# Optimization experiments

Measured on AMD Instinct MI355X. Metric: run time of the kernel, lower is better.

The kernel has to match this reference:

```python
import jax, jax.numpy as jnp
import numpy as np

N = 50000          # nodes
E = 800000         # edges (avg degree 16)
F = 128            # in_dim = num_hidden*heads = pred_dim
H = 4              # attention heads per layer
D = 32             # num_hidden (per-head dim)
R = 11             # rel_num
L = 2              # num_layers
SCALE = float(1.0 / np.sqrt(D))


def setup_inputs() -> dict:
    key = jax.random.key(0)
    ks = jax.random.split(key, 16)
    inputs = jax.random.normal(ks[0], (N, F), jnp.float32)
    edge_types = jax.random.randint(ks[1], (E,), 0, R)
    src = jax.random.randint(ks[2], (E,), 0, N)
    dst = jax.random.randint(ks[3], (E,), 0, N)
    centrality = jax.random.uniform(ks[4], (N,), jnp.float32)
    rel_emb = jax.random.normal(ks[5], (R, F), jnp.float32) * 0.1
    # stacked per-layer projection weights (both layers have F -> H*D = F)
    Wq = jax.random.normal(ks[6], (L, F, H * D), jnp.float32) * 0.05
    Wk = jax.random.normal(ks[7], (L, F, H * D), jnp.float32) * 0.05
    Wv = jax.random.normal(ks[8], (L, F, H * D), jnp.float32) * 0.05
    We = jax.random.normal(ks[9], (L, F, H * D), jnp.float32) * 0.05
    bq = jnp.zeros((L, H * D), jnp.float32)
    bk = jnp.zeros((L, H * D), jnp.float32)
    bv = jnp.zeros((L, H * D), jnp.float32)
    be = jnp.zeros((L, H * D), jnp.float32)
    W_out = jax.random.normal(ks[10], (H * D, 1), jnp.float32) * 0.05
    b_out = jnp.zeros((1,), jnp.float32)
    gamma = jnp.ones((1,), jnp.float32)
    beta = jnp.zeros((1,), jnp.float32)
    return {"inputs": inputs, "edge_types": edge_types, "src": src, "dst": dst,
            "centrality": centrality, "rel_emb": rel_emb,
            "Wq": Wq, "bq": bq, "Wk": Wk, "bk": bk, "Wv": Wv, "bv": bv,
            "We": We, "be": be, "W_out": W_out, "b_out": b_out,
            "gamma": gamma, "beta": beta}


def _segment_softmax(score, dst, n):
    # score: [E, H]; softmax over incoming edges of each dst node
    m = jax.ops.segment_max(score, dst, num_segments=n)          # [N, H]
    ex = jnp.exp(score - m[dst])                                  # [E, H]
    s = jax.ops.segment_sum(ex, dst, num_segments=n)              # [N, H]
    return ex / (s[dst] + 1e-9)


def reference(inputs, edge_types, src, dst, centrality, rel_emb,
              Wq, bq, Wk, bk, Wv, bv, We, be, W_out, b_out, gamma, beta):
    h = inputs                                   # [N, F]
    ef = rel_emb[edge_types]                     # [E, pred_dim] relational edge embedding
    for l in range(L):
        q = (h @ Wq[l] + bq[l]).reshape(N, H, D)
        k = (h @ Wk[l] + bk[l]).reshape(N, H, D)
        v = (h @ Wv[l] + bv[l]).reshape(N, H, D)
        e = (ef @ We[l] + be[l]).reshape(E, H, D)
        # edge_mode="add": edge features added to keys/values on each edge
        ke = k[src] + e                           # [E, H, D]
        score = jnp.sum(q[dst] * ke, axis=-1) * SCALE   # [E, H]
        attn = _segment_softmax(score, dst, N)          # [E, H]
        msg = attn[:, :, None] * (v[src] + e)           # [E, H, D]
        agg = jax.ops.segment_sum(msg, dst, num_segments=N)  # [N, H, D]
        # identity residual (in_dim == H*D) + ELU activation
        h = jax.nn.elu(agg.reshape(N, H * D) + h)
    logits = h @ W_out + b_out                    # [N, 1]
    logits = jax.nn.relu((centrality * gamma + beta)[:, None] * logits)
    return logits
```

## Files before the change

kernel.cpp:

```cpp
#include <hip/hip_runtime.h>
#include <hip/hip_bf16.h>
#include <math.h>

#define SCALE_C 0.17677669529663687f
#define CAPP 64

typedef short bf16x8 __attribute__((ext_vector_type(8)));
typedef float f32x4 __attribute__((ext_vector_type(4)));
typedef _Float16 h16x2 __attribute__((ext_vector_type(2)));

__device__ __forceinline__ h16x2 bch2(unsigned u) { return __builtin_bit_cast(h16x2, u); }


__global__ __launch_bounds__(256) void prep_scatter_k(
    const float* __restrict__ Wq, const float* __restrict__ Wk, const float* __restrict__ Wv,
    __hip_bfloat16* __restrict__ wf,
    const float* __restrict__ rel_emb, const float* __restrict__ We, const float* __restrict__ be,
    _Float16* __restrict__ re, int R, int reb,
    const int* __restrict__ dst, const int* __restrict__ src, const int* __restrict__ etype,
    int E, int* __restrict__ cnt, int* __restrict__ bins) {
  int b = blockIdx.x;
  if (b < 48) {
    int tid = b * 256 + threadIdx.x;
    int lane = tid & 63;
    int frag = tid >> 6;
    int ks = frag & 3;
    int ct = (frag >> 2) & 7;
    int mat = frag >> 5;
    int l = mat / 3, m = mat % 3;
    const float* W = ((m == 0) ? Wq : (m == 1) ? Wk : Wv) + (size_t)l * 128 * 128;
    int nn = ct * 16 + (lane & 15);
    int k0 = ks * 32 + (lane >> 4) * 8;
    __hip_bfloat16 tmp[8];
    #pragma unroll
    for (int j = 0; j < 8; ++j) tmp[j] = __float2bfloat16(W[(size_t)(k0 + j) * 128 + nn]);
    *(uint4*)&wf[(size_t)frag * 64 * 8 + (size_t)lane * 8] = *(const uint4*)tmp;
  } else if (b < 48 + reb) {
    int idx = (b - 48) * 256 + threadIdx.x;
    int tot = 2 * R * 128;
    if (idx >= tot) return;
    int c = idx & 127;
    int r = (idx >> 7) % R;
    int l = idx / (R * 128);
    const float* W = We + (size_t)l * 128 * 128;
    float acc = be[l * 128 + c];
    #pragma unroll 4
    for (int kk = 0; kk < 128; ++kk) acc += rel_emb[r * 128 + kk] * W[kk * 128 + c];
    re[idx] = (_Float16)acc;
  } else {
    int e = (b - 48 - reb) * 256 + threadIdx.x;
    if (e < E) {
      int d = dst[e];
      int pos = atomicAdd(&cnt[d], 1);
      if (pos < CAPP) bins[(d << 6) + pos] = src[e] | (etype[e] << 20);
    }
  }
}


__device__ __forceinline__ void qkv_body(
    const float* __restrict__ Xf, const __hip_bfloat16* __restrict__ Xb,
    const __hip_bfloat16* __restrict__ wf,
    const float* __restrict__ bq, const float* __restrict__ bk, const float* __restrict__ bv,
    _Float16* __restrict__ qo, _Float16* __restrict__ kvo, int n, int bid) {
  __shared__ _Float16 kvt[2][32][264];
  int wid = threadIdx.x >> 6;
  int lane = threadIdx.x & 63;
  int row0 = bid * 64 + wid * 32;
  if (row0 >= n) return;
  int cl = lane & 15;
  int quad = lane >> 4;

  bf16x8 afrag[2][4];
  #pragma unroll
  for (int s = 0; s < 2; ++s) {
    int arow = row0 + s * 16 + cl;
    bool av = arow < n;
    if (Xb) {
      const __hip_bfloat16* xr = Xb + (size_t)arow * 128 + quad * 8;
      #pragma unroll
      for (int ks = 0; ks < 4; ++ks) {
        uint4 raw = av ? *(const uint4*)(xr + ks * 32) : make_uint4(0, 0, 0, 0);
        afrag[s][ks] = __builtin_bit_cast(bf16x8, raw);
      }
    } else {
      const float* xr = Xf + (size_t)arow * 128 + quad * 8;
      #pragma unroll
      for (int ks = 0; ks < 4; ++ks) {
        float4 x0 = av ? *(const float4*)(xr + ks * 32)     : make_float4(0.f, 0.f, 0.f, 0.f);
        float4 x1 = av ? *(const float4*)(xr + ks * 32 + 4) : make_float4(0.f, 0.f, 0.f, 0.f);
        union { bf16x8 v; __hip_bfloat16 h[8]; } fu;
        fu.h[0] = __float2bfloat16(x0.x); fu.h[1] = __float2bfloat16(x0.y);
        fu.h[2] = __float2bfloat16(x0.z); fu.h[3] = __float2bfloat16(x0.w);
        fu.h[4] = __float2bfloat16(x1.x); fu.h[5] = __float2bfloat16(x1.y);
        fu.h[6] = __float2bfloat16(x1.z); fu.h[7] = __float2bfloat16(x1.w);
        afrag[s][ks] = fu.v;
      }
    }
  }
  const uint4* wfu = (const uint4*)wf;

  #pragma unroll
  for (int ct = 0; ct < 8; ++ct) {
    f32x4 a0 = {0.f, 0.f, 0.f, 0.f}, a1 = {0.f, 0.f, 0.f, 0.f};
    #pragma unroll
    for (int ks = 0; ks < 4; ++ks) {
      uint4 braw = wfu[((size_t)ct * 4 + ks) * 64 + lane];
      bf16x8 bfr = __builtin_bit_cast(bf16x8, braw);
      a0 = __builtin_amdgcn_mfma_f32_16x16x32_bf16(afrag[0][ks], bfr, a0, 0, 0, 0);
      a1 = __builtin_amdgcn_mfma_f32_16x16x32_bf16(afrag[1][ks], bfr, a1, 0, 0, 0);
    }
    int c = ct * 16 + cl;
    float bb = bq[c];
    #pragma unroll
    for (int r = 0; r < 4; ++r) {
      kvt[wid][quad * 4 + r][c]      = (_Float16)((a0[r] + bb) * SCALE_C);
      kvt[wid][16 + quad * 4 + r][c] = (_Float16)((a1[r] + bb) * SCALE_C);
    }
  }
  {
    const uint4* tsrc = (const uint4*)&kvt[wid][0][0];
    #pragma unroll
    for (int it = 0; it < 8; ++it) {
      int idx = it * 64 + lane;
      int row = idx >> 4, g = idx & 15;
      if (row0 + row < n)
        *(uint4*)&qo[((size_t)(row0 + row)) * 128 + g * 8] = tsrc[row * 33 + g];
    }
  }

  #pragma unroll
  for (int m = 1; m <= 2; ++m) {
    const float* bias = (m == 1) ? bk : bv;
    #pragma unroll
    for (int ct = 0; ct < 8; ++ct) {
      f32x4 a0 = {0.f, 0.f, 0.f, 0.f}, a1 = {0.f, 0.f, 0.f, 0.f};
      #pragma unroll
      for (int ks = 0; ks < 4; ++ks) {
        uint4 braw = wfu[((size_t)(m * 8 + ct) * 4 + ks) * 64 + lane];
        bf16x8 bfr = __builtin_bit_cast(bf16x8, braw);
        a0 = __builtin_amdgcn_mfma_f32_16x16x32_bf16(afrag[0][ks], bfr, a0, 0, 0, 0);
        a1 = __builtin_amdgcn_mfma_f32_16x16x32_bf16(afrag[1][ks], bfr, a1, 0, 0, 0);
      }
      int c = ct * 16 + cl;
      float bb = bias[c];
      int p = 8 * (c >> 2) + (c & 3) + ((m == 2) ? 4 : 0);
      #pragma unroll
      for (int r = 0; r < 4; ++r) {
        kvt[wid][quad * 4 + r][p]      = (_Float16)(a0[r] + bb);
        kvt[wid][16 + quad * 4 + r][p] = (_Float16)(a1[r] + bb);
      }
    }
  }
  {
    const uint4* tsrc = (const uint4*)&kvt[wid][0][0];
    #pragma unroll
    for (int it = 0; it < 16; ++it) {
      int idx = it * 64 + lane;
      int row = idx >> 5, off = idx & 31;
      if (row0 + row < n)
        *(uint4*)&kvo[((size_t)(row0 + row)) * 256 + off * 8] = tsrc[row * 33 + off];
    }
  }
}

__global__ __launch_bounds__(128) void qkv1_k(
    const float* __restrict__ Xf, const __hip_bfloat16* __restrict__ wf,
    const float* __restrict__ bq, const float* __restrict__ bk, const float* __restrict__ bv,
    _Float16* __restrict__ qo, _Float16* __restrict__ kvo, int n) {
  qkv_body(Xf, nullptr, wf, bq, bk, bv, qo, kvo, n, blockIdx.x);
}

__global__ __launch_bounds__(128) void qkv2_k(
    const __hip_bfloat16* __restrict__ Xb, const __hip_bfloat16* __restrict__ wf,
    const float* __restrict__ bq, const float* __restrict__ bk, const float* __restrict__ bv,
    _Float16* __restrict__ qo, _Float16* __restrict__ kvo, int n) {
  qkv_body(nullptr, Xb, wf, bq, bk, bv, qo, kvo, n, blockIdx.x);
}


__global__ __launch_bounds__(256) void edge_k(
    const _Float16* __restrict__ qb, const _Float16* __restrict__ kv,
    const _Float16* __restrict__ re,
    const int* __restrict__ bins, const int* __restrict__ cnt,
    const float* __restrict__ h_in_f, const __hip_bfloat16* __restrict__ h_in_b,
    __hip_bfloat16* __restrict__ h_out_b,
    const float* __restrict__ Wout, const float* __restrict__ bout,
    const float* __restrict__ cent, const float* __restrict__ gamma,
    const float* __restrict__ beta, float* __restrict__ outp, int n) {
  int node = blockIdx.x * 4 + (threadIdx.x >> 6);
  if (node >= n) return;
  int lane = threadIdx.x & 63;
  int j = lane & 15;
  int quarter = lane >> 4;
  int deg = cnt[node];
  deg = deg < CAPP ? deg : CAPP;
  uint nm1 = (uint)(n - 1);

  int pkrow = bins[(node << 6) + lane];

  uint4 qraw = *((const uint4*)(qb + ((size_t)node << 7)) + j);
  h16x2 q01 = bch2(qraw.x), q23 = bch2(qraw.y), q45 = bch2(qraw.z), q67 = bch2(qraw.w);
  float qa0 = (float)q01.x, qa1 = (float)q01.y;
  float qa2 = (float)q23.x, qa3 = (float)q23.y;
  float qa4 = (float)q45.x, qa5 = (float)q45.y;
  float qa6 = (float)q67.x, qa7 = (float)q67.y;

  float ssum = 0.f;
  float acc0 = 0.f, acc1 = 0.f, acc2 = 0.f, acc3 = 0.f;
  float acc4 = 0.f, acc5 = 0.f, acc6 = 0.f, acc7 = 0.f;

  int nit = (deg + 3) >> 2;
  nit = (nit + 1) & ~1;

  const uint4* kvb  = (const uint4*)kv + (uint)(j * 2);
  const uint4* rebp = (const uint4*)re + (uint)j;

  auto loadstage = [&](int pk, uint4& r0, uint4& r1, uint4& rr) {
    uint s = (uint)pk & 0xFFFFFu; s = s < nm1 ? s : nm1;
    uint t = (uint)pk >> 20;
    const uint4* kp = kvb + s * 32u;
    r0 = kp[0];
    r1 = kp[1];
    rr = rebp[t * 16u];
  };
  auto accum = [&](uint4 r0, uint4 r1, uint4 rr, int eidx) {
    h16x2 r01 = bch2(rr.x), r23 = bch2(rr.y), r45 = bch2(rr.z), r67 = bch2(rr.w);
    h16x2 kr01 = bch2(r0.x) + r01;
    h16x2 kr23 = bch2(r0.y) + r23;
    h16x2 kr45 = bch2(r1.x) + r45;
    h16x2 kr67 = bch2(r1.y) + r67;
    h16x2 vr01 = bch2(r0.z) + r01;
    h16x2 vr23 = bch2(r0.w) + r23;
    h16x2 vr45 = bch2(r1.z) + r45;
    h16x2 vr67 = bch2(r1.w) + r67;
    float pA = qa0 * (float)kr01.x;
    pA += qa1 * (float)kr01.y;
    pA += qa2 * (float)kr23.x;
    pA += qa3 * (float)kr23.y;
    float pB = qa4 * (float)kr45.x;
    pB += qa5 * (float)kr45.y;
    pB += qa6 * (float)kr67.x;
    pB += qa7 * (float)kr67.y;
    float p = pA + pB;
    p += __shfl_xor(p, 1);
    p += __shfl_xor(p, 2);
    float w = (eidx < deg) ? __expf(p) : 0.f;
    ssum += w;
    acc0 += w * (float)vr01.x;
    acc1 += w * (float)vr01.y;
    acc2 += w * (float)vr23.x;
    acc3 += w * (float)vr23.y;
    acc4 += w * (float)vr45.x;
    acc5 += w * (float)vr45.y;
    acc6 += w * (float)vr67.x;
    acc7 += w * (float)vr67.y;
  };

  uint4 a0, a1, ar, b0, b1, br;
  loadstage(__shfl(pkrow, quarter), a0, a1, ar);
  loadstage(__shfl(pkrow, 4 + quarter), b0, b1, br);

  for (int i = 0; i < nit; i += 2) {
    bool more = (i + 2) < nit;
    int pkA2 = 0, pkB2 = 0;
    if (more) {
      pkA2 = __shfl(pkrow, (4 * i + 8 + quarter) & 63);
      pkB2 = __shfl(pkrow, (4 * i + 12 + quarter) & 63);
    }
    accum(a0, a1, ar, 4 * i + quarter);
    if (more) loadstage(pkA2, a0, a1, ar);
    accum(b0, b1, br, 4 * i + 4 + quarter);
    if (more) loadstage(pkB2, b0, b1, br);
  }

  ssum += __shfl_xor(ssum, 16); ssum += __shfl_xor(ssum, 32);
  acc0 += __shfl_xor(acc0, 16); acc0 += __shfl_xor(acc0, 32);
  acc1 += __shfl_xor(acc1, 16); acc1 += __shfl_xor(acc1, 32);
  acc2 += __shfl_xor(acc2, 16); acc2 += __shfl_xor(acc2, 32);
  acc3 += __shfl_xor(acc3, 16); acc3 += __shfl_xor(acc3, 32);
  acc4 += __shfl_xor(acc4, 16); acc4 += __shfl_xor(acc4, 32);
  acc5 += __shfl_xor(acc5, 16); acc5 += __shfl_xor(acc5, 32);
  acc6 += __shfl_xor(acc6, 16); acc6 += __shfl_xor(acc6, 32);
  acc7 += __shfl_xor(acc7, 16); acc7 += __shfl_xor(acc7, 32);
  if (quarter != 0) return;

  float inv = __builtin_amdgcn_rcpf(ssum + 1e-9f);
  float4 h0, h1;
  if (h_in_b) {
    uint4 hraw = *((const uint4*)(h_in_b + ((size_t)node << 7)) + j);
    h0.x = __uint_as_float(hraw.x << 16); h0.y = __uint_as_float(hraw.x & 0xffff0000u);
    h0.z = __uint_as_float(hraw.y << 16); h0.w = __uint_as_float(hraw.y & 0xffff0000u);
    h1.x = __uint_as_float(hraw.z << 16); h1.y = __uint_as_float(hraw.z & 0xffff0000u);
    h1.z = __uint_as_float(hraw.w << 16); h1.w = __uint_as_float(hraw.w & 0xffff0000u);
  } else {
    const float4* hrow = (const float4*)h_in_f + ((uint)node * 32u + (uint)(j * 2));
    h0 = hrow[0]; h1 = hrow[1];
  }
  float x0 = acc0 * inv + h0.x;
  float x1 = acc1 * inv + h0.y;
  float x2 = acc2 * inv + h0.z;
  float x3 = acc3 * inv + h0.w;
  float x4 = acc4 * inv + h1.x;
  float x5 = acc5 * inv + h1.y;
  float x6 = acc6 * inv + h1.z;
  float x7 = acc7 * inv + h1.w;
  x0 = x0 > 0.f ? x0 : __expf(x0) - 1.f;
  x1 = x1 > 0.f ? x1 : __expf(x1) - 1.f;
  x2 = x2 > 0.f ? x2 : __expf(x2) - 1.f;
  x3 = x3 > 0.f ? x3 : __expf(x3) - 1.f;
  x4 = x4 > 0.f ? x4 : __expf(x4) - 1.f;
  x5 = x5 > 0.f ? x5 : __expf(x5) - 1.f;
  x6 = x6 > 0.f ? x6 : __expf(x6) - 1.f;
  x7 = x7 > 0.f ? x7 : __expf(x7) - 1.f;
  if (outp == nullptr) {
    union { uint4 u; __hip_bfloat16 hh[8]; } P;
    P.hh[0] = __float2bfloat16(x0); P.hh[1] = __float2bfloat16(x1);
    P.hh[2] = __float2bfloat16(x2); P.hh[3] = __float2bfloat16(x3);
    P.hh[4] = __float2bfloat16(x4); P.hh[5] = __float2bfloat16(x5);
    P.hh[6] = __float2bfloat16(x6); P.hh[7] = __float2bfloat16(x7);
    *((uint4*)(h_out_b + ((size_t)node << 7)) + j) = P.u;
  } else {
    const float4* wrow = (const float4*)Wout + (uint)(j * 2);
    float4 w0 = wrow[0], w1 = wrow[1];
    float pp = x0 * w0.x + x1 * w0.y + x2 * w0.z + x3 * w0.w
             + x4 * w1.x + x5 * w1.y + x6 * w1.z + x7 * w1.w;
    pp += __shfl_xor(pp, 1);
    pp += __shfl_xor(pp, 2);
    pp += __shfl_xor(pp, 4);
    pp += __shfl_xor(pp, 8);
    if (lane == 0) {
      float lg = pp + bout[0];
      lg *= (cent[node] * gamma[0] + beta[0]);
      outp[node] = fmaxf(lg, 0.f);
    }
  }
}


extern "C" void kernel_launch(void* const* d_in, const int* in_sizes, int n_in,
                              void* d_out, int out_size, void* d_ws, size_t ws_size,
                              hipStream_t stream) {
  const float* inputs  = (const float*)d_in[0];
  const int*   etype   = (const int*)d_in[1];
  const int*   src     = (const int*)d_in[2];
  const int*   dst     = (const int*)d_in[3];
  const float* cent    = (const float*)d_in[4];
  const float* rel_emb = (const float*)d_in[5];
  const float* Wq      = (const float*)d_in[6];
  const float* bq      = (const float*)d_in[7];
  const float* Wk      = (const float*)d_in[8];
  const float* bk      = (const float*)d_in[9];
  const float* Wv      = (const float*)d_in[10];
  const float* bv      = (const float*)d_in[11];
  const float* We      = (const float*)d_in[12];
  const float* be      = (const float*)d_in[13];
  const float* Wout    = (const float*)d_in[14];
  const float* bout    = (const float*)d_in[15];
  const float* gamma   = (const float*)d_in[16];
  const float* beta    = (const float*)d_in[17];
  float* out = (float*)d_out;

  const int N = in_sizes[0] / 128;
  const int E = in_sizes[1];
  const int R = in_sizes[5] / 128;

  _Float16* re = (_Float16*)d_ws;
  __hip_bfloat16* hb = (__hip_bfloat16*)(re + 2 * (size_t)R * 128);
  _Float16* qb = (_Float16*)(hb + (size_t)N * 128);
  _Float16* kv = qb + (size_t)N * 128;
  __hip_bfloat16* wf = (__hip_bfloat16*)(kv + (size_t)N * 256);
  int* cnt  = (int*)(wf + 6 * 16384);
  int* bins = cnt + N;

  hipMemsetAsync(cnt, 0, (size_t)N * sizeof(int), stream);

  int reb = (2 * R * 128 + 255) / 256;
  int SB  = (E + 255) / 256;
  prep_scatter_k<<<48 + reb + SB, 256, 0, stream>>>(Wq, Wk, Wv, wf, rel_emb, We, be, re, R, reb,
                                                    dst, src, etype, E, cnt, bins);

  int QB = (N + 63) / 64;
  int eb = (N + 3) / 4;
  qkv1_k<<<QB, 128, 0, stream>>>(inputs, wf, bq, bk, bv, qb, kv, N);
  edge_k<<<eb, 256, 0, stream>>>(qb, kv, re, bins, cnt,
                                 inputs, nullptr, hb,
                                 Wout, bout, cent, gamma, beta, nullptr, N);
  qkv2_k<<<QB, 128, 0, stream>>>(hb, wf + (size_t)3 * 16384,
                                 bq + 128, bk + 128, bv + 128, qb, kv, N);
  edge_k<<<eb, 256, 0, stream>>>(qb, kv, re + (size_t)R * 128, bins, cnt,
                                 nullptr, hb, nullptr,
                                 Wout, bout, cent, gamma, beta, out, N);
}
```

Before: 311.0 us.

## Split QKV projection across three waves and de-interleave KV layout

The QKV kernel now stages a 32-row input tile in shared memory and gives each of three waves one projection (Q, K or V). Previously each wave computed all three for its own 32 rows. The KV buffer layout changes from interleaved per-4-element K/V groups to contiguous K then V halves, and the edge gather loads kp[0] and kp[16] to match. In the edge kernel, loads of the bins, q and residual h rows become nontemporal and are issued early, and bin loads are masked by degree. The aim is more parallel waves and earlier latency hiding. In exchange the gather needs two separate 16-byte loads per edge that sit far apart in memory, and the QKV kernel adds a shared-memory staging pass with a barrier.

```diff
diff --git a/kernel.cpp b/kernel.cpp
--- a/kernel.cpp
+++ b/kernel.cpp
@@ -8,8 +8,14 @@
 typedef short bf16x8 __attribute__((ext_vector_type(8)));
 typedef float f32x4 __attribute__((ext_vector_type(4)));
 typedef _Float16 h16x2 __attribute__((ext_vector_type(2)));
+typedef unsigned u32x4 __attribute__((ext_vector_type(4)));
 
 __device__ __forceinline__ h16x2 bch2(unsigned u) { return __builtin_bit_cast(h16x2, u); }
+
+__device__ __forceinline__ uint4 nt_load16(const void* p) {
+  u32x4 v = __builtin_nontemporal_load((const u32x4*)p);
+  return __builtin_bit_cast(uint4, v);
+}
 
 
 __global__ __launch_bounds__(256) void prep_scatter_k(
@@ -63,115 +69,96 @@
     const __hip_bfloat16* __restrict__ wf,
     const float* __restrict__ bq, const float* __restrict__ bk, const float* __restrict__ bv,
     _Float16* __restrict__ qo, _Float16* __restrict__ kvo, int n, int bid) {
-  __shared__ _Float16 kvt[2][32][264];
-  int wid = threadIdx.x >> 6;
-  int lane = threadIdx.x & 63;
-  int row0 = bid * 64 + wid * 32;
+  __shared__ __attribute__((aligned(16))) __hip_bfloat16 xs[32][136];
+  __shared__ __attribute__((aligned(16))) _Float16 ot[3][32][136];
+  int tid = threadIdx.x;
+  int wid = tid >> 6;
+  int lane = tid & 63;
+  int row0 = bid * 32;
   if (row0 >= n) return;
+
+  for (int idx = tid; idx < 512; idx += 192) {
+    int row = idx >> 4, g = idx & 15;
+    union { uint4 u; __hip_bfloat16 h[8]; } P;
+    P.u = make_uint4(0, 0, 0, 0);
+    if (row0 + row < n) {
+      if (Xb) {
+        P.u = *(const uint4*)(Xb + (size_t)(row0 + row) * 128 + g * 8);
+      } else {
+        const float* xr = Xf + (size_t)(row0 + row) * 128 + g * 8;
+        float4 x0 = *(const float4*)xr;
+        float4 x1 = *(const float4*)(xr + 4);
+        P.h[0] = __float2bfloat16(x0.x); P.h[1] = __float2bfloat16(x0.y);
+        P.h[2] = __float2bfloat16(x0.z); P.h[3] = __float2bfloat16(x0.w);
+        P.h[4] = __float2bfloat16(x1.x); P.h[5] = __float2bfloat16(x1.y);
+        P.h[6] = __float2bfloat16(x1.z); P.h[7] = __float2bfloat16(x1.w);
+      }
+    }
+    *(uint4*)&xs[row][g * 8] = P.u;
+  }
+  __syncthreads();
+
   int cl = lane & 15;
   int quad = lane >> 4;
 
   bf16x8 afrag[2][4];
   #pragma unroll
-  for (int s = 0; s < 2; ++s) {
-    int arow = row0 + s * 16 + cl;
-    bool av = arow < n;
-    if (Xb) {
-      const __hip_bfloat16* xr = Xb + (size_t)arow * 128 + quad * 8;
-      #pragma unroll
-      for (int ks = 0; ks < 4; ++ks) {
-        uint4 raw = av ? *(const uint4*)(xr + ks * 32) : make_uint4(0, 0, 0, 0);
-        afrag[s][ks] = __builtin_bit_cast(bf16x8, raw);
-      }
-    } else {
-      const float* xr = Xf + (size_t)arow * 128 + quad * 8;
-      #pragma unroll
-      for (int ks = 0; ks < 4; ++ks) {
-        float4 x0 = av ? *(const float4*)(xr + ks * 32)     : make_float4(0.f, 0.f, 0.f, 0.f);
-        float4 x1 = av ? *(const float4*)(xr + ks * 32 + 4) : make_float4(0.f, 0.f, 0.f, 0.f);
-        union { bf16x8 v; __hip_bfloat16 h[8]; } fu;
-        fu.h[0] = __float2bfloat16(x0.x); fu.h[1] = __float2bfloat16(x0.y);
-        fu.h[2] = __float2bfloat16(x0.z); fu.h[3] = __float2bfloat16(x0.w);
-        fu.h[4] = __float2bfloat16(x1.x); fu.h[5] = __float2bfloat16(x1.y);
-        fu.h[6] = __float2bfloat16(x1.z); fu.h[7] = __float2bfloat16(x1.w);
-        afrag[s][ks] = fu.v;
-      }
-    }
-  }
+  for (int s = 0; s < 2; ++s)
+    #pragma unroll
+    for (int ks = 0; ks < 4; ++ks)
+      afrag[s][ks] = *(const bf16x8*)&xs[s * 16 + cl][quad * 8 + ks * 32];
+
   const uint4* wfu = (const uint4*)wf;
+  const float* bias = (wid == 0) ? bq : (wid == 1) ? bk : bv;
+  float scl = (wid == 0) ? SCALE_C : 1.0f;
 
   #pragma unroll
   for (int ct = 0; ct < 8; ++ct) {
     f32x4 a0 = {0.f, 0.f, 0.f, 0.f}, a1 = {0.f, 0.f, 0.f, 0.f};
     #pragma unroll
     for (int ks = 0; ks < 4; ++ks) {
-      uint4 braw = wfu[((size_t)ct * 4 + ks) * 64 + lane];
+      uint4 braw = wfu[((size_t)(wid * 8 + ct) * 4 + ks) * 64 + lane];
       bf16x8 bfr = __builtin_bit_cast(bf16x8, braw);
       a0 = __builtin_amdgcn_mfma_f32_16x16x32_bf16(afrag[0][ks], bfr, a0, 0, 0, 0);
       a1 = __builtin_amdgcn_mfma_f32_16x16x32_bf16(afrag[1][ks], bfr, a1, 0, 0, 0);
     }
     int c = ct * 16 + cl;
-    float bb = bq[c];
+    float bb = bias[c];
     #pragma unroll
     for (int r = 0; r < 4; ++r) {
-      kvt[wid][quad * 4 + r][c]      = (_Float16)((a0[r] + bb) * SCALE_C);
-      kvt[wid][16 + quad * 4 + r][c] = (_Float16)((a1[r] + bb) * SCALE_C);
-    }
-  }
-  {
-    const uint4* tsrc = (const uint4*)&kvt[wid][0][0];
+      ot[wid][quad * 4 + r][c]      = (_Float16)((a0[r] + bb) * scl);
+      ot[wid][16 + quad * 4 + r][c] = (_Float16)((a1[r] + bb) * scl);
+    }
+  }
+
+  if (wid == 0) {
     #pragma unroll
     for (int it = 0; it < 8; ++it) {
       int idx = it * 64 + lane;
       int row = idx >> 4, g = idx & 15;
       if (row0 + row < n)
-        *(uint4*)&qo[((size_t)(row0 + row)) * 128 + g * 8] = tsrc[row * 33 + g];
-    }
-  }
-
-  #pragma unroll
-  for (int m = 1; m <= 2; ++m) {
-    const float* bias = (m == 1) ? bk : bv;
-    #pragma unroll
-    for (int ct = 0; ct < 8; ++ct) {
-      f32x4 a0 = {0.f, 0.f, 0.f, 0.f}, a1 = {0.f, 0.f, 0.f, 0.f};
-      #pragma unroll
-      for (int ks = 0; ks < 4; ++ks) {
-        uint4 braw = wfu[((size_t)(m * 8 + ct) * 4 + ks) * 64 + lane];
-        bf16x8 bfr = __builtin_bit_cast(bf16x8, braw);
-        a0 = __builtin_amdgcn_mfma_f32_16x16x32_bf16(afrag[0][ks], bfr, a0, 0, 0, 0);
-        a1 = __builtin_amdgcn_mfma_f32_16x16x32_bf16(afrag[1][ks], bfr, a1, 0, 0, 0);
-      }
-      int c = ct * 16 + cl;
-      float bb = bias[c];
-      int p = 8 * (c >> 2) + (c & 3) + ((m == 2) ? 4 : 0);
-      #pragma unroll
-      for (int r = 0; r < 4; ++r) {
-        kvt[wid][quad * 4 + r][p]      = (_Float16)(a0[r] + bb);
-        kvt[wid][16 + quad * 4 + r][p] = (_Float16)(a1[r] + bb);
-      }
-    }
-  }
-  {
-    const uint4* tsrc = (const uint4*)&kvt[wid][0][0];
-    #pragma unroll
-    for (int it = 0; it < 16; ++it) {
+        *(uint4*)&qo[(size_t)(row0 + row) * 128 + g * 8] = *(const uint4*)&ot[0][row][g * 8];
+    }
+  } else {
+    int off = (wid == 1) ? 0 : 128;
+    #pragma unroll
+    for (int it = 0; it < 8; ++it) {
       int idx = it * 64 + lane;
-      int row = idx >> 5, off = idx & 31;
+      int row = idx >> 4, g = idx & 15;
       if (row0 + row < n)
-        *(uint4*)&kvo[((size_t)(row0 + row)) * 256 + off * 8] = tsrc[row * 33 + off];
-    }
-  }
-}
-
-__global__ __launch_bounds__(128) void qkv1_k(
+        *(uint4*)&kvo[(size_t)(row0 + row) * 256 + off + g * 8] = *(const uint4*)&ot[wid][row][g * 8];
+    }
+  }
+}
+
+__global__ __launch_bounds__(192) void qkv1_k(
     const float* __restrict__ Xf, const __hip_bfloat16* __restrict__ wf,
     const float* __restrict__ bq, const float* __restrict__ bk, const float* __restrict__ bv,
     _Float16* __restrict__ qo, _Float16* __restrict__ kvo, int n) {
   qkv_body(Xf, nullptr, wf, bq, bk, bv, qo, kvo, n, blockIdx.x);
 }
 
-__global__ __launch_bounds__(128) void qkv2_k(
+__global__ __launch_bounds__(192) void qkv2_k(
     const __hip_bfloat16* __restrict__ Xb, const __hip_bfloat16* __restrict__ wf,
     const float* __restrict__ bq, const float* __restrict__ bk, const float* __restrict__ bv,
     _Float16* __restrict__ qo, _Float16* __restrict__ kvo, int n) {
@@ -197,9 +184,27 @@
   deg = deg < CAPP ? deg : CAPP;
   uint nm1 = (uint)(n - 1);
 
-  int pkrow = bins[(node << 6) + lane];
-
-  uint4 qraw = *((const uint4*)(qb + ((size_t)node << 7)) + j);
+  int pkrow = (lane < deg) ? __builtin_nontemporal_load(bins + (node << 6) + lane) : 0;
+
+  uint4 qraw = nt_load16((const uint4*)(qb + ((size_t)node << 7)) + j);
+
+  float4 h0, h1;
+  if (h_in_b) {
+    uint4 hraw = nt_load16((const uint4*)(h_in_b + ((size_t)node << 7)) + j);
+    h0.x = __uint_as_float(hraw.x << 16); h0.y = __uint_as_float(hraw.x & 0xffff0000u);
+    h0.z = __uint_as_float(hraw.y << 16); h0.w = __uint_as_float(hraw.y & 0xffff0000u);
+    h1.x = __uint_as_float(hraw.z << 16); h1.y = __uint_as_float(hraw.z & 0xffff0000u);
+    h1.z = __uint_as_float(hraw.w << 16); h1.w = __uint_as_float(hraw.w & 0xffff0000u);
+  } else {
+    const float4* hrow = (const float4*)h_in_f + ((uint)node * 32u + (uint)(j * 2));
+    uint4 t0 = nt_load16(hrow);
+    uint4 t1 = nt_load16(hrow + 1);
+    h0.x = __uint_as_float(t0.x); h0.y = __uint_as_float(t0.y);
+    h0.z = __uint_as_float(t0.z); h0.w = __uint_as_float(t0.w);
+    h1.x = __uint_as_float(t1.x); h1.y = __uint_as_float(t1.y);
+    h1.z = __uint_as_float(t1.z); h1.w = __uint_as_float(t1.w);
+  }
+
   h16x2 q01 = bch2(qraw.x), q23 = bch2(qraw.y), q45 = bch2(qraw.z), q67 = bch2(qraw.w);
   float qa0 = (float)q01.x, qa1 = (float)q01.y;
   float qa2 = (float)q23.x, qa3 = (float)q23.y;
@@ -213,27 +218,27 @@
   int nit = (deg + 3) >> 2;
   nit = (nit + 1) & ~1;
 
-  const uint4* kvb  = (const uint4*)kv + (uint)(j * 2);
+  const uint4* kvb  = (const uint4*)kv + (uint)j;
   const uint4* rebp = (const uint4*)re + (uint)j;
 
-  auto loadstage = [&](int pk, uint4& r0, uint4& r1, uint4& rr) {
+  auto loadstage = [&](int pk, uint4& rk, uint4& rv, uint4& rr) {
     uint s = (uint)pk & 0xFFFFFu; s = s < nm1 ? s : nm1;
     uint t = (uint)pk >> 20;
     const uint4* kp = kvb + s * 32u;
-    r0 = kp[0];
-    r1 = kp[1];
+    rk = kp[0];
+    rv = kp[16];
     rr = rebp[t * 16u];
   };
-  auto accum = [&](uint4 r0, uint4 r1, uint4 rr, int eidx) {
+  auto accum = [&](uint4 rk, uint4 rv, uint4 rr, int eidx) {
     h16x2 r01 = bch2(rr.x), r23 = bch2(rr.y), r45 = bch2(rr.z), r67 = bch2(rr.w);
-    h16x2 kr01 = bch2(r0.x) + r01;
-    h16x2 kr23 = bch2(r0.y) + r23;
-    h16x2 kr45 = bch2(r1.x) + r45;
-    h16x2 kr67 = bch2(r1.y) + r67;
-    h16x2 vr01 = bch2(r0.z) + r01;
-    h16x2 vr23 = bch2(r0.w) + r23;
-    h16x2 vr45 = bch2(r1.z) + r45;
-    h16x2 vr67 = bch2(r1.w) + r67;
+    h16x2 kr01 = bch2(rk.x) + r01;
+    h16x2 kr23 = bch2(rk.y) + r23;
+    h16x2 kr45 = bch2(rk.z) + r45;
+    h16x2 kr67 = bch2(rk.w) + r67;
+    h16x2 vr01 = bch2(rv.x) + r01;
+    h16x2 vr23 = bch2(rv.y) + r23;
+    h16x2 vr45 = bch2(rv.z) + r45;
+    h16x2 vr67 = bch2(rv.w) + r67;
     float pA = qa0 * (float)kr01.x;
     pA += qa1 * (float)kr01.y;
     pA += qa2 * (float)kr23.x;
@@ -286,17 +291,6 @@
   if (quarter != 0) return;
 
   float inv = __builtin_amdgcn_rcpf(ssum + 1e-9f);
-  float4 h0, h1;
-  if (h_in_b) {
-    uint4 hraw = *((const uint4*)(h_in_b + ((size_t)node << 7)) + j);
-    h0.x = __uint_as_float(hraw.x << 16); h0.y = __uint_as_float(hraw.x & 0xffff0000u);
-    h0.z = __uint_as_float(hraw.y << 16); h0.w = __uint_as_float(hraw.y & 0xffff0000u);
-    h1.x = __uint_as_float(hraw.z << 16); h1.y = __uint_as_float(hraw.z & 0xffff0000u);
-    h1.z = __uint_as_float(hraw.w << 16); h1.w = __uint_as_float(hraw.w & 0xffff0000u);
-  } else {
-    const float4* hrow = (const float4*)h_in_f + ((uint)node * 32u + (uint)(j * 2));
-    h0 = hrow[0]; h1 = hrow[1];
-  }
   float x0 = acc0 * inv + h0.x;
   float x1 = acc1 * inv + h0.y;
   float x2 = acc2 * inv + h0.z;
@@ -380,13 +374,13 @@
   prep_scatter_k<<<48 + reb + SB, 256, 0, stream>>>(Wq, Wk, Wv, wf, rel_emb, We, be, re, R, reb,
                                                     dst, src, etype, E, cnt, bins);
 
-  int QB = (N + 63) / 64;
+  int QB = (N + 31) / 32;
   int eb = (N + 3) / 4;
-  qkv1_k<<<QB, 128, 0, stream>>>(inputs, wf, bq, bk, bv, qb, kv, N);
+  qkv1_k<<<QB, 192, 0, stream>>>(inputs, wf, bq, bk, bv, qb, kv, N);
   edge_k<<<eb, 256, 0, stream>>>(qb, kv, re, bins, cnt,
                                  inputs, nullptr, hb,
                                  Wout, bout, cent, gamma, beta, nullptr, N);
-  qkv2_k<<<QB, 128, 0, stream>>>(hb, wf + (size_t)3 * 16384,
+  qkv2_k<<<QB, 192, 0, stream>>>(hb, wf + (size_t)3 * 16384,
                                  bq + 128, bk + 128, bv + 128, qb, kv, N);
   edge_k<<<eb, 256, 0, stream>>>(qb, kv, re + (size_t)R * 128, bins, cnt,
                                  nullptr, hb, nullptr,
```

Measured after the change: 301.3 us. 3.1% less time.
